# Optimization experiments

Hardware: AMD Instinct MI355X
Metric: run time of the kernel (lower is better)

## Reference

```python
import jax, jax.numpy as jnp
from jax import lax
import numpy as np

B, S, D, H = 64, 256, 1024, 1024
NEG = -1e9


def setup_inputs() -> dict:
    key = jax.random.key(0)
    ks = jax.random.split(key, 8)
    sd = 1.0 / np.sqrt(D)
    sh = 1.0 / np.sqrt(H + 1)
    return {
        "lstm_features": jax.random.normal(ks[0], (B, S, D), jnp.float32),
        "mask": jnp.ones((B, S), jnp.int32),
        "Wl": jax.random.normal(ks[1], (D, H), jnp.float32) * sd,
        "bl": jnp.zeros((H,), jnp.float32),
        "Wr": jax.random.normal(ks[2], (D, H), jnp.float32) * sd,
        "br": jnp.zeros((H,), jnp.float32),
        "Wbil": jax.random.normal(ks[3], (H + 1, H + 1), jnp.float32) * sh,
        "bbil": jnp.zeros((), jnp.float32),
    }


def _span_scores(lstm_features, Wl, bl, Wr, br, Wbil, bbil):
    # left/right MLPs: Linear + LeakyReLU(0.1) (dropout=0 at inference)
    lefts = jax.nn.leaky_relu(lstm_features @ Wl + bl, 0.1)   # [B,S,H]
    rights = jax.nn.leaky_relu(lstm_features @ Wr + br, 0.1)  # [B,S,H]
    ones = jnp.ones(lefts.shape[:-1] + (1,), lefts.dtype)
    l1 = jnp.concatenate([lefts, ones], axis=-1)   # [B,S,H+1] (use_input_biases=True)
    r1 = jnp.concatenate([rights, ones], axis=-1)
    # bilinear: l1 @ W @ r1^T + bias  -> [B,S,S]
    return jnp.einsum('bsh,hg,btg->bst', l1, Wbil, r1) + bbil


def _cky(scores):
    """CKY over one [S,S] score matrix. chart[i,j]=scores[i,j]+max_s chart[i,s]+chart[s+1,j];
    singleton spans score 0. Returns (chart, best-split table)."""
    n = scores.shape[0]
    idx = jnp.arange(n)
    m = jnp.arange(n - 1)  # split offsets
    chart0 = jnp.zeros((n, n), scores.dtype)
    split0 = jnp.zeros((n, n), jnp.int32)

    def step(carry, w):
        chart, split = carry
        j = idx + w
        jc = jnp.clip(j, 0, n - 1)
        li = jnp.clip(idx[:, None] + m[None, :], 0, n - 1)       # left end
        ri = jnp.clip(idx[:, None] + m[None, :] + 1, 0, n - 1)   # right start
        cand = chart[idx[:, None], li] + chart[ri, jc[:, None]]  # [n, n-1]
        valid = (m[None, :] < w) & (j[:, None] < n)
        cand = jnp.where(valid, cand, NEG)
        val = scores[idx, jc] + jnp.max(cand, axis=1)
        bsplit = (idx + jnp.argmax(cand, axis=1)).astype(jnp.int32)
        ok = j < n
        chart = chart.at[idx, jc].set(jnp.where(ok, val, chart[idx, jc]))
        split = split.at[idx, jc].set(jnp.where(ok, bsplit, split[idx, jc]))
        return (chart, split), None

    (chart, split), _ = lax.scan(step, (chart0, split0), jnp.arange(1, n))
    return chart, split


def _backtrack(split):
    """Extract the n-1 internal spans of the best tree (fixed-size stack, jit-safe)."""
    n = split.shape[0]
    stack = jnp.full((2 * n, 2), -1, jnp.int32).at[0].set(jnp.array([0, n - 1], jnp.int32))
    out = jnp.zeros((n, 2), jnp.int32)

    def body(t, state):
        def do_pop(st):
            stack, top, out, cnt = st
            ij = stack[top - 1]
            i, j = ij[0], ij[1]
            top = top - 1
            out = out.at[cnt].set(ij)
            cnt = cnt + 1
            s = split[i, j]
            stack = stack.at[top].set(jnp.stack([i, s]))          # left child
            top = top + (s > i).astype(jnp.int32)
            stack = stack.at[top].set(jnp.stack([s + 1, j]))      # right child
            top = top + (j > s + 1).astype(jnp.int32)
            return (stack, top, out, cnt)
        return lax.cond(state[1] > 0, do_pop, lambda s: s, state)

    state = (stack, jnp.int32(1), out, jnp.int32(0))
    _, _, out, _ = lax.fori_loop(0, n - 1, body, state)
    return out  # [n,2] (lefts, rights), zero-padded like torch.zeros in original


def reference(lstm_features, mask, Wl, bl, Wr, br, Wbil, bbil):
    scores = _span_scores(lstm_features, Wl, bl, Wr, br, Wbil, bbil)  # [B,S,S]
    _, split = jax.vmap(_cky)(scores)
    spans = jax.vmap(_backtrack)(split)  # [B,S,2]
    ret_lefts = spans[..., 0].astype(jnp.int64)
    ret_rights = spans[..., 1].astype(jnp.int64)
    return ret_lefts, ret_rights
```

## Files before the change

### kernel.cpp

```cpp
#include <hip/hip_runtime.h>
#include <cstdint>


#define Bb 64
#define Ss 256
#define Dd 1024
#define Hh 1024

typedef __attribute__((ext_vector_type(8))) _Float16 f16x8;
typedef __attribute__((ext_vector_type(4))) float f32x4;

__device__ __forceinline__ void split2(float x, unsigned short& h,
                                       unsigned short& l) {
  _Float16 hh = (_Float16)x;
  _Float16 ll = (_Float16)(x - (float)hh);
  h = __builtin_bit_cast(unsigned short, hh);
  l = __builtin_bit_cast(unsigned short, ll);
}

__global__ __launch_bounds__(256) void splitw_kernel(
    const float* __restrict__ W, int ldw, unsigned short* __restrict__ O,
    long long plane) {
  int idx = blockIdx.x * 256 + threadIdx.x;
  int n = idx >> 10, k = idx & 1023;
  float x = W[(long long)k * ldw + n];
  unsigned short h, l;
  split2(x, h, l);
  O[idx] = h;
  O[plane + idx] = l;
}

__global__ __launch_bounds__(256) void bilvec_kernel(
    const float* __restrict__ Wbil, float* __restrict__ brow,
    float* __restrict__ bcol, float* __restrict__ corner) {
  int i = blockIdx.x * 256 + threadIdx.x;
  brow[i] = Wbil[1024 * 1025 + i];
  bcol[i] = Wbil[i * 1025 + 1024];
  if (i == 0) corner[0] = Wbil[1024 * 1025 + 1024];
}

__device__ __forceinline__ void pack8(char* dst, const unsigned short* v) {
  uint4 u;
  u.x = (unsigned)v[0] | ((unsigned)v[1] << 16);
  u.y = (unsigned)v[2] | ((unsigned)v[3] << 16);
  u.z = (unsigned)v[4] | ((unsigned)v[5] << 16);
  u.w = (unsigned)v[6] | ((unsigned)v[7] << 16);
  *(uint4*)dst = u;
}

__device__ __forceinline__ void split_store16f(const float* xs, char* lds,
                                               int base, int wa0, int wa1) {
  unsigned short hs[16], ls[16];
#pragma unroll
  for (int i = 0; i < 16; ++i) split2(xs[i], hs[i], ls[i]);
  pack8(&lds[base + wa0], hs);
  pack8(&lds[base + wa1], hs + 8);
  pack8(&lds[base + 8192 + wa0], ls);
  pack8(&lds[base + 8192 + wa1], ls + 8);
}

#define MFMA4(afv, bh, blv, accs, nf)                                        \
  {                                                                          \
    _Pragma("unroll") for (int mf = 0; mf < 4; ++mf) accs[mf][nf] =          \
        __builtin_amdgcn_mfma_f32_16x16x32_f16(afv[0][mf], bh,               \
                                               accs[mf][nf], 0, 0, 0);       \
    _Pragma("unroll") for (int mf = 0; mf < 4; ++mf) accs[mf][nf] =          \
        __builtin_amdgcn_mfma_f32_16x16x32_f16(afv[0][mf], blv,              \
                                               accs[mf][nf], 0, 0, 0);       \
    _Pragma("unroll") for (int mf = 0; mf < 4; ++mf) accs[mf][nf] =          \
        __builtin_amdgcn_mfma_f32_16x16x32_f16(afv[1][mf], bh,               \
                                               accs[mf][nf], 0, 0, 0);       \
    _Pragma("unroll") for (int mf = 0; mf < 4; ++mf) accs[mf][nf] =          \
        __builtin_amdgcn_mfma_f32_16x16x32_f16(afv[1][mf], blv,              \
                                               accs[mf][nf], 0, 0, 0);       \
  }

template <bool LEAKY>
__global__ __launch_bounds__(256, 3) void gemm_mfma_kernel(
    const float* __restrict__ A, const unsigned short* __restrict__ Bsp,
    long long bplane, float* __restrict__ C0, float* __restrict__ C1,
    const float* __restrict__ bias0, const float* __restrict__ bias1) {
  const int m0 = blockIdx.y * 128;
  const int n0 = blockIdx.x * 128;
  __shared__ __align__(16) char lds[32768];
  const int t = threadIdx.x;
  const int L = t & 63, w = t >> 6, q = L >> 4, l15 = L & 15;

  const int ar = t >> 1, ah = t & 1;
  const float* aptr = A + (long long)(m0 + ar) * 1024 + ah * 16;
  const int phiA = ((ar >> 1) ^ (ar >> 3)) & 3;
  const int wa0 = ar * 64 + (((2 * ah + 0) ^ phiA) << 4);
  const int wa1 = ar * 64 + (((2 * ah + 1) ^ phiA) << 4);

  int offA0[4], offB0[4];
#pragma unroll
  for (int f = 0; f < 4; ++f) {
    int rowa = ((w & 1) << 6) + (f << 4) + l15;
    offA0[f] = rowa * 64 + ((q ^ (((rowa >> 1) ^ (rowa >> 3)) & 3)) << 4);
    int rowb = ((w >> 1) << 6) + (f << 4) + l15;
    offB0[f] =
        16384 + rowb * 64 + ((q ^ (((rowb >> 1) ^ (rowb >> 3)) & 3)) << 4);
  }

  f32x4 acc[4][4];
#pragma unroll
  for (int i = 0; i < 4; ++i)
#pragma unroll
    for (int j = 0; j < 4; ++j) acc[i][j] = (f32x4){0.f, 0.f, 0.f, 0.f};

  for (int k0 = 0; k0 < 1024; k0 += 32) {
#pragma unroll
    for (int j = 0; j < 4; ++j) {
      int fc = t + (j << 8);
      int s = fc >> 9, r = (fc >> 2) & 127, sc = fc & 3;
      const unsigned short* bs = Bsp + s * bplane;
      uint4 bv =
          *(const uint4*)(bs + (long long)(n0 + r) * 1024 + k0 + (sc << 3));
      int phi = ((r >> 1) ^ (r >> 3)) & 3;
      *(uint4*)&lds[16384 + s * 8192 + r * 64 + ((sc ^ phi) << 4)] = bv;
    }
    {
      float4 a0 = *(const float4*)(aptr + k0);
      float4 a1 = *(const float4*)(aptr + k0 + 4);
      float4 a2 = *(const float4*)(aptr + k0 + 8);
      float4 a3 = *(const float4*)(aptr + k0 + 12);
      float xs[16] = {a0.x, a0.y, a0.z, a0.w, a1.x, a1.y, a1.z, a1.w,
                      a2.x, a2.y, a2.z, a2.w, a3.x, a3.y, a3.z, a3.w};
      split_store16f(xs, lds, 0, wa0, wa1);
    }
    __syncthreads();
    f16x8 af[2][4];
#pragma unroll
    for (int s = 0; s < 2; ++s)
#pragma unroll
      for (int f = 0; f < 4; ++f)
        af[s][f] = *(const f16x8*)&lds[s * 8192 + offA0[f]];
#pragma unroll
    for (int nf = 0; nf < 4; ++nf) {
      f16x8 bh = *(const f16x8*)&lds[offB0[nf]];
      f16x8 bl = *(const f16x8*)&lds[8192 + offB0[nf]];
      MFMA4(af, bh, bl, acc, nf);
    }
    __syncthreads();
  }

  const bool isR = (n0 >= 1024);
  float* Co = isR ? C1 : C0;
  const float* bp = isR ? bias1 : bias0;
  const int nc0 = n0 & 1023;
#pragma unroll
  for (int nf = 0; nf < 4; ++nf) {
    int col = nc0 + ((w >> 1) << 6) + (nf << 4) + l15;
    float bz = bp[col];
#pragma unroll
    for (int mf = 0; mf < 4; ++mf) {
#pragma unroll
      for (int r = 0; r < 4; ++r) {
        int row = m0 + ((w & 1) << 6) + (mf << 4) + (q << 2) + r;
        float x = acc[mf][nf][r] + bz;
        if (LEAKY) x = (x > 0.f) ? x : 0.1f * x;
        Co[(long long)row * 1024 + col] = x;
      }
    }
  }
}

__global__ __launch_bounds__(256, 3) void gemmnt_mfma_kernel(
    const float* __restrict__ A, const float* __restrict__ B,
    float* __restrict__ C, const float* __restrict__ rowAdd,
    const float* __restrict__ scal) {
  const int bz = blockIdx.z;
  A += (long long)bz * 256 * 1024;
  B += (long long)bz * 256 * 1024;
  C += (long long)bz * 256 * 256;
  const int m0 = blockIdx.y * 128;
  const int n0 = blockIdx.x * 128;
  __shared__ __align__(16) char lds[32768];
  const int t = threadIdx.x;
  const int L = t & 63, w = t >> 6, q = L >> 4, l15 = L & 15;

  const int ar = t >> 1, ah = t & 1;
  const float* aptr = A + (long long)(m0 + ar) * 1024 + ah * 16;
  const float* bptr = B + (long long)(n0 + ar) * 1024 + ah * 16;
  const int phiA = ((ar >> 1) ^ (ar >> 3)) & 3;
  const int wa0 = ar * 64 + (((2 * ah + 0) ^ phiA) << 4);
  const int wa1 = ar * 64 + (((2 * ah + 1) ^ phiA) << 4);

  int offA0[4], offB0[4];
#pragma unroll
  for (int f = 0; f < 4; ++f) {
    int rowa = ((w & 1) << 6) + (f << 4) + l15;
    offA0[f] = rowa * 64 + ((q ^ (((rowa >> 1) ^ (rowa >> 3)) & 3)) << 4);
    int rowb = ((w >> 1) << 6) + (f << 4) + l15;
    offB0[f] =
        16384 + rowb * 64 + ((q ^ (((rowb >> 1) ^ (rowb >> 3)) & 3)) << 4);
  }

  f32x4 acc[4][4];
#pragma unroll
  for (int i = 0; i < 4; ++i)
#pragma unroll
    for (int j = 0; j < 4; ++j) acc[i][j] = (f32x4){0.f, 0.f, 0.f, 0.f};

  for (int k0 = 0; k0 < 1024; k0 += 32) {
    {
      float4 a0 = *(const float4*)(aptr + k0);
      float4 a1 = *(const float4*)(aptr + k0 + 4);
      float4 a2 = *(const float4*)(aptr + k0 + 8);
      float4 a3 = *(const float4*)(aptr + k0 + 12);
      float xs[16] = {a0.x, a0.y, a0.z, a0.w, a1.x, a1.y, a1.z, a1.w,
                      a2.x, a2.y, a2.z, a2.w, a3.x, a3.y, a3.z, a3.w};
      split_store16f(xs, lds, 0, wa0, wa1);
      float4 b0 = *(const float4*)(bptr + k0);
      float4 b1 = *(const float4*)(bptr + k0 + 4);
      float4 b2 = *(const float4*)(bptr + k0 + 8);
      float4 b3 = *(const float4*)(bptr + k0 + 12);
      float ys[16] = {b0.x, b0.y, b0.z, b0.w, b1.x, b1.y, b1.z, b1.w,
                      b2.x, b2.y, b2.z, b2.w, b3.x, b3.y, b3.z, b3.w};
      split_store16f(ys, lds, 16384, wa0, wa1);
    }
    __syncthreads();
    f16x8 af[2][4];
#pragma unroll
    for (int s = 0; s < 2; ++s)
#pragma unroll
      for (int f = 0; f < 4; ++f)
        af[s][f] = *(const f16x8*)&lds[s * 8192 + offA0[f]];
#pragma unroll
    for (int nf = 0; nf < 4; ++nf) {
      f16x8 bh = *(const f16x8*)&lds[offB0[nf]];
      f16x8 bl = *(const f16x8*)&lds[8192 + offB0[nf]];
      MFMA4(af, bh, bl, acc, nf);
    }
    __syncthreads();
  }

  const float sc_add = scal[0];
#pragma unroll
  for (int mf = 0; mf < 4; ++mf) {
#pragma unroll
    for (int r = 0; r < 4; ++r) {
      int row = m0 + ((w & 1) << 6) + (mf << 4) + (q << 2) + r;
      float radd = sc_add + rowAdd[(long long)bz * 256 + row];
#pragma unroll
      for (int nf = 0; nf < 4; ++nf) {
        int col = n0 + ((w >> 1) << 6) + (nf << 4) + l15;
        C[(long long)row * 256 + col] = acc[mf][nf][r] + radd;
      }
    }
  }
}

__global__ __launch_bounds__(64) void colvec_kernel(
    const float* __restrict__ lefts, const float* __restrict__ bcol,
    const float* __restrict__ corner, float* __restrict__ tmpb) {
  int row = blockIdx.x;
  int lane = threadIdx.x;
  const float* a = lefts + (long long)row * Hh;
  float s = 0.f;
#pragma unroll
  for (int h = lane; h < Hh; h += 64) s = fmaf(a[h], bcol[h], s);
#pragma unroll
  for (int off = 32; off > 0; off >>= 1) s += __shfl_down(s, off, 64);
  if (lane == 0) tmpb[row] = s + corner[0];
}

__global__ __launch_bounds__(1024) void cky_kernel(
    const float* __restrict__ scores,
    uint8_t* __restrict__ Sws,
    int* __restrict__ out)
{
  const int b = blockIdx.x;
  const int t = threadIdx.x;
  const int n = Ss;
  const float* sc = scores + (long long)b * n * n;
  uint8_t* SP = Sws + (long long)b * 32896;

  __shared__ float Dch[32896];
  __shared__ float pv[2][2048];
  __shared__ uint8_t pmv[2][2048];
  __shared__ int stk[256];

  const int offT[10] = {0,    256,  511,  765,  1018,
                        1270, 1521, 1771, 2020, 2268};

  if (t < n) {
    out[b * n + t] = 0;
    out[Bb * n + b * n + t] = 0;
    Dch[t] = 0.f;
  }

  float PS[10];
  PS[0] = 0.f;
#pragma unroll
  for (int w = 1; w <= 9; ++w) {
    int ic = t;
    if (ic > 255 - w) ic = 255 - w;
    PS[w] = sc[ic * 257 + w];
  }
  asm volatile("s_waitcnt lgkmcnt(0)\n\ts_barrier" ::: "memory");

#pragma unroll
  for (int w = 1; w <= 9; ++w) {
    const int nv = n - w;
    if (t < nv) {
      float bb = Dch[offT[w - 1] + t + 1];
      int bm = 0;
#pragma unroll
      for (int m = 1; m < 9; ++m) {
        if (m >= w) break;
        float c = Dch[offT[m] + t] + Dch[offT[w - 1 - m] + t + m + 1];
        if (c > bb) { bb = c; bm = m; }
      }
      const int off = w * 256 - ((w * (w - 1)) >> 1);
      Dch[off + t] = PS[w] + bb;
      SP[off + t] = (uint8_t)bm;
    }
    asm volatile("s_waitcnt lgkmcnt(0)\n\ts_barrier" ::: "memory");
  }

  auto run_b = [&](int W0b, int pbuf) {
    const int cnv = n - W0b - 4;
    int jb, gb, u, delta, lgGHL, SLOTG;
    if (cnv > 128) {
      const int p = t >> 7;
      jb = 3 - (p >> 1);
      gb = 1 - (p & 1);
      u = t & 127;
      delta = 128;
      lgGHL = 1;
      SLOTG = 256;
    } else {
      const int wid = t >> 6;
      jb = 3 - (wid >> 2);
      gb = 3 - (wid & 3);
      u = t & 63;
      delta = (cnv > 64) ? 64 : 0;
      lgGHL = 2;
      SLOTG = 128;
    }
    const int Wb = W0b + 4 + jb;
    const int nvb = n - Wb;
    int cnt = W0b - jb - 4;
    if (cnt < 0) cnt = 0;
    const int per = (cnt + (1 << lgGHL) - 1) >> lgGHL;
    const int mlo = jb + 4;
    int ml = mlo + gb * per;
    int mh = mlo + cnt;
    {
      int e = ml + per;
      if (e < mh) mh = e;
    }
    float b0 = -3.0e38f, b1 = -3.0e38f;
    int m0i = ml, m1i = ml;
    if (u < nvb && ml < mh) {
      int al = ml * n - ((ml * (ml - 1)) >> 1) + u;
      const int kr = Wb - 1 - ml;
      int ar = kr * n - ((kr * (kr - 1)) >> 1) + u + ml + 1;
      int dl = n - ml;
      int dr = n - Wb + ml + 1;
      if (delta) {
#pragma unroll 2
        for (int m = ml; m < mh; ++m) {
          float l0 = Dch[al], l1 = Dch[al + delta];
          float r0 = Dch[ar], r1 = Dch[ar + delta];
          float c0 = l0 + r0, c1 = l1 + r1;
          if (c0 > b0) { b0 = c0; m0i = m; }
          if (c1 > b1) { b1 = c1; m1i = m; }
          al += dl;
          ar -= dr;
          --dl;
          ++dr;
        }
      } else {
#pragma unroll 4
        for (int m = ml; m < mh; ++m) {
          float c = Dch[al] + Dch[ar];
          if (c > b0) { b0 = c; m0i = m; }
          al += dl;
          ar -= dr;
          --dl;
          ++dr;
        }
      }
    }
    const int slot = jb * 512 + gb * SLOTG + u;
    pv[pbuf][slot] = b0;
    pmv[pbuf][slot] = (uint8_t)m0i;
    if (delta) {
      pv[pbuf][slot + delta] = b1;
      pmv[pbuf][slot + delta] = (uint8_t)m1i;
    }
  };

  run_b(6, 0);
  asm volatile("s_waitcnt lgkmcnt(0)\n\ts_barrier" ::: "memory");

  const int wv = t >> 6, lane = t & 63;
  const int tcell = 61 * wv + lane;

  float scA[4];
#pragma unroll
  for (int j = 0; j < 4; ++j) {
    const int Wn = 10 + j;
    int ic = tcell;
    if (ic > 255 - Wn) ic = 255 - Wn;
    if (ic < 0) ic = 0;
    scA[j] = sc[ic * 257 + Wn];
  }

  for (int s = 3; s <= 64; ++s) {
    const int W0 = 4 * s - 2;
    const int nv1 = n - W0;
    const int pb = s & 1, po = pb ^ 1;
    const int nb = (nv1 + 60) / 61;

    float P4[4] = {0.f, 0.f, 0.f, 0.f};
    if (s < 64 && wv < nb) {
#pragma unroll
      for (int j = 0; j < 4; ++j) {
        const int Wn = W0 + 4 + j;
        int ic = tcell;
        if (ic > 255 - Wn) ic = 255 - Wn;
        if (ic < 0) ic = 0;
        P4[j] = sc[ic * 257 + Wn];
      }
    }

    if (wv < nb) {
      const int tc = (tcell < nv1) ? tcell : (nv1 - 1);
      const float* pvo = pv[po];
      const uint8_t* pmo = pmv[po];
      int GHa, SGa;
      if (nv1 > 128) { GHa = 2; SGa = 256; } else { GHa = 4; SGa = 128; }
      int offPB[4], offCB[4];
#pragma unroll
      for (int d = 0; d < 4; ++d) {
        const int dg = W0 - 4 + d;
        offPB[d] = dg * 256 - ((dg * (dg - 1)) >> 1);
        const int cg = W0 + d;
        offCB[d] = cg * 256 - ((cg * (cg - 1)) >> 1);
      }
      float VAL0, VAL1, VAL2, VAL3;
      float SH01, SH02, SH03, SH11, SH12, SH21;
      {
        const int W = W0;
        float bb = Dch[offPB[3] + tc + 1];
        int bm = 0;
#pragma unroll
        for (int dm = 1; dm < 4; ++dm) {
          const int m = dm;
          float c = Dch[offT[m] + tc] + Dch[offPB[3 - dm] + tc + m + 1];
          if (c > bb) { bb = c; bm = m; }
        }
#pragma unroll
        for (int g = 0; g < 4; ++g) {
          if (g >= GHa) break;
          const int sl = g * SGa + tc;
          float x = pvo[sl];
          if (x > bb) { bb = x; bm = pmo[sl]; }
        }
#pragma unroll
        for (int dr = 3; dr >= 0; --dr) {
          const int r = dr;
          const int m = W - 1 - r;
          float right = (r == 0) ? 0.f : Dch[offT[r] + tc + W - r];
          float c = Dch[offPB[3 - dr] + tc] + right;
          if (c > bb) { bb = c; bm = m; }
        }
        VAL0 = scA[0] + bb;
        if (tcell < nv1) {
          Dch[offCB[0] + tcell] = VAL0;
          SP[offCB[0] + tcell] = (uint8_t)bm;
        }
        SH01 = __shfl_down(VAL0, 1, 64);
        SH02 = __shfl_down(VAL0, 2, 64);
        SH03 = __shfl_down(VAL0, 3, 64);
      }
      {
        const int W = W0 + 1;
        float bb = SH01;
        int bm = 0;
#pragma unroll
        for (int dm = 0; dm < 4; ++dm) {
          const int m = 1 + dm;
          float c = Dch[offT[m] + tc] + Dch[offPB[3 - dm] + tc + m + 1];
          if (c > bb) { bb = c; bm = m; }
        }
#pragma unroll
        for (int g = 0; g < 4; ++g) {
          if (g >= GHa) break;
          const int sl = 512 + g * SGa + tc;
          float x = pvo[sl];
          if (x > bb) { bb = x; bm = pmo[sl]; }
        }
#pragma unroll
        for (int dr = 3; dr >= 0; --dr) {
          const int r = 1 + dr;
          const int m = W - 1 - r;
          float c = Dch[offPB[3 - dr] + tc] + Dch[offT[r] + tc + W - r];
          if (c > bb) { bb = c; bm = m; }
        }
        if (VAL0 > bb) { bb = VAL0; bm = W - 1; }
        VAL1 = scA[1] + bb;
        if (lane <= 62 && tcell < nv1 - 1) {
          Dch[offCB[1] + tcell] = VAL1;
          SP[offCB[1] + tcell] = (uint8_t)bm;
        }
        SH11 = __shfl_down(VAL1, 1, 64);
        SH12 = __shfl_down(VAL1, 2, 64);
      }
      {
        const int W = W0 + 2;
        float bb = SH11;
        int bm = 0;
        {
          float c = Dch[offT[1] + tc] + SH02;
          if (c > bb) { bb = c; bm = 1; }
        }
#pragma unroll
        for (int dm = 0; dm < 4; ++dm) {
          const int m = 2 + dm;
          float c = Dch[offT[m] + tc] + Dch[offPB[3 - dm] + tc + m + 1];
          if (c > bb) { bb = c; bm = m; }
        }
#pragma unroll
        for (int g = 0; g < 4; ++g) {
          if (g >= GHa) break;
          const int sl = 1024 + g * SGa + tc;
          float x = pvo[sl];
          if (x > bb) { bb = x; bm = pmo[sl]; }
        }
#pragma unroll
        for (int dr = 3; dr >= 0; --dr) {
          const int r = 2 + dr;
          const int m = W - 1 - r;
          float c = Dch[offPB[3 - dr] + tc] + Dch[offT[r] + tc + W - r];
          if (c > bb) { bb = c; bm = m; }
        }
        {
          float c = VAL0 + Dch[offT[1] + tc + W - 1];
          if (c > bb) { bb = c; bm = W - 2; }
        }
        if (VAL1 > bb) { bb = VAL1; bm = W - 1; }
        VAL2 = scA[2] + bb;
        if (lane <= 61 && tcell < nv1 - 2) {
          Dch[offCB[2] + tcell] = VAL2;
          SP[offCB[2] + tcell] = (uint8_t)bm;
        }
        SH21 = __shfl_down(VAL2, 1, 64);
      }
      {
        const int W = W0 + 3;
        float bb = SH21;
        int bm = 0;
        {
          float c = Dch[offT[1] + tc] + SH12;
          if (c > bb) { bb = c; bm = 1; }
        }
        {
          float c = Dch[offT[2] + tc] + SH03;
          if (c > bb) { bb = c; bm = 2; }
        }
#pragma unroll
        for (int dm = 0; dm < 4; ++dm) {
          const int m = 3 + dm;
          float c = Dch[offT[m] + tc] + Dch[offPB[3 - dm] + tc + m + 1];
          if (c > bb) { bb = c; bm = m; }
        }
#pragma unroll
        for (int g = 0; g < 4; ++g) {
          if (g >= GHa) break;
          const int sl = 1536 + g * SGa + tc;
          float x = pvo[sl];
          if (x > bb) { bb = x; bm = pmo[sl]; }
        }
#pragma unroll
        for (int dr = 3; dr >= 0; --dr) {
          const int r = 3 + dr;
          const int m = W - 1 - r;
          float c = Dch[offPB[3 - dr] + tc] + Dch[offT[r] + tc + W - r];
          if (c > bb) { bb = c; bm = m; }
        }
        {
          float c = VAL0 + Dch[offT[2] + tc + W - 2];
          if (c > bb) { bb = c; bm = W - 3; }
        }
        {
          float c = VAL1 + Dch[offT[1] + tc + W - 1];
          if (c > bb) { bb = c; bm = W - 2; }
        }
        if (VAL2 > bb) { bb = VAL2; bm = W - 1; }
        VAL3 = scA[3] + bb;
        if (lane <= 60 && tcell < nv1 - 3) {
          Dch[offCB[3] + tcell] = VAL3;
          SP[offCB[3] + tcell] = (uint8_t)bm;
        }
      }
    }

    if (s < 64) run_b(W0, pb);

    asm volatile("s_waitcnt lgkmcnt(0)\n\ts_barrier" ::: "memory");
#pragma unroll
    for (int j = 0; j < 4; ++j) scA[j] = P4[j];
  }

  asm volatile("s_waitcnt vmcnt(0) lgkmcnt(0)\n\ts_barrier" ::: "memory");
  uint8_t* spl = (uint8_t*)Dch;
  for (int idx = t; idx < 32896; idx += 1024) spl[idx] = SP[idx];
  asm volatile("s_waitcnt vmcnt(0) lgkmcnt(0)\n\ts_barrier" ::: "memory");
  if (t == 0) {
    int top = 0;
    stk[top++] = (0 << 16) | (n - 1);
    int cnt = 0;
    for (int step = 0; step < n - 1; ++step) {
      if (top > 0) {
        int ij = stk[--top];
        int ii = ij >> 16, jj = ij & 0xffff;
        out[b * n + cnt] = ii;
        out[Bb * n + b * n + cnt] = jj;
        ++cnt;
        int k = jj - ii;
        int s2 = ii + (int)spl[k * n - ((k * (k - 1)) >> 1) + ii];
        stk[top] = (ii << 16) | s2;
        if (s2 > ii) ++top;
        stk[top] = ((s2 + 1) << 16) | jj;
        if (jj > s2 + 1) ++top;
      }
    }
  }
}

extern "C" void kernel_launch(void* const* d_in, const int* in_sizes, int n_in,
                              void* d_out, int out_size, void* d_ws,
                              size_t ws_size, hipStream_t stream) {
  const float* X = (const float*)d_in[0];
  const float* Wl = (const float*)d_in[2];
  const float* bl = (const float*)d_in[3];
  const float* Wr = (const float*)d_in[4];
  const float* br = (const float*)d_in[5];
  const float* Wbil = (const float*)d_in[6];
  const float* bbil = (const float*)d_in[7];
  int* out = (int*)d_out;

  float* ws = (float*)d_ws;
  float* lefts = ws;
  float* rights = lefts + 16777216;
  float* tmpA = rights + 16777216;
  float* scoresP = tmpA + 16777216;
  float* tmpb = scoresP + 4194304;
  float* browp = tmpb + 16384;
  float* bcolp = browp + 1024;
  float* cornerp = bcolp + 1024;
  unsigned short* Wlrt = (unsigned short*)(cornerp + 4);
  unsigned short* Wct = Wlrt + 2LL * 2097152;
  uint8_t* SPp = (uint8_t*)(Wct + 2LL * 1048576);

  splitw_kernel<<<dim3(4096), 256, 0, stream>>>(Wl, 1024, Wlrt, 2097152);
  splitw_kernel<<<dim3(4096), 256, 0, stream>>>(Wr, 1024, Wlrt + 1048576,
                                                2097152);
  splitw_kernel<<<dim3(4096), 256, 0, stream>>>(Wbil, 1025, Wct, 1048576);
  bilvec_kernel<<<dim3(4), 256, 0, stream>>>(Wbil, browp, bcolp, cornerp);

  dim3 gLR(16, 128);
  gemm_mfma_kernel<true><<<gLR, 256, 0, stream>>>(X, Wlrt, 2097152LL, lefts,
                                                  rights, bl, br);

  colvec_kernel<<<dim3(16384), 64, 0, stream>>>(lefts, bcolp, cornerp, tmpb);

  dim3 gA(8, 128);
  gemm_mfma_kernel<false><<<gA, 256, 0, stream>>>(lefts, Wct, 1048576LL, tmpA,
                                                  tmpA, browp, browp);

  dim3 g3(2, 2, 64);
  gemmnt_mfma_kernel<<<g3, 256, 0, stream>>>(tmpA, rights, scoresP, tmpb,
                                             bbil);

  cky_kernel<<<dim3(Bb), dim3(1024), 0, stream>>>(scoresP, SPp, out);
}
```

Baseline: 943.7 us.

## Prefetch next K-tile in GEMMs via direct global-to-LDS loads and double buffering

In the projection GEMM, the pre-split fp16 B tiles now go straight from global memory to LDS through global_load_lds into a double-buffered region. The fp32 A tile for the next k-step is prefetched into registers while MFMAs run on the current one. The bilinear GEMM gets the same register prefetch for both operands. Plain __syncthreads is replaced with explicit waitcnt plus s_barrier so load latency overlaps compute. LDS use grows from 32KB to 48KB, which may lower occupancy relative to the launch-bounds target of 3 blocks per CU.

```diff
diff --git a/kernel.cpp b/kernel.cpp
--- a/kernel.cpp
+++ b/kernel.cpp
@@ -16,6 +16,12 @@
   _Float16 ll = (_Float16)(x - (float)hh);
   h = __builtin_bit_cast(unsigned short, hh);
   l = __builtin_bit_cast(unsigned short, ll);
+}
+
+__device__ __forceinline__ void gl_lds16(const void* g, void* l) {
+  __builtin_amdgcn_global_load_lds(
+      (const __attribute__((address_space(1))) void*)g,
+      (__attribute__((address_space(3))) void*)l, 16, 0, 0);
 }
 
 __global__ __launch_bounds__(256) void splitw_kernel(
@@ -82,7 +88,7 @@
     const float* __restrict__ bias0, const float* __restrict__ bias1) {
   const int m0 = blockIdx.y * 128;
   const int n0 = blockIdx.x * 128;
-  __shared__ __align__(16) char lds[32768];
+  __shared__ __align__(16) char lds[49152];
   const int t = threadIdx.x;
   const int L = t & 63, w = t >> 6, q = L >> 4, l15 = L & 15;
 
@@ -98,8 +104,21 @@
     int rowa = ((w & 1) << 6) + (f << 4) + l15;
     offA0[f] = rowa * 64 + ((q ^ (((rowa >> 1) ^ (rowa >> 3)) & 3)) << 4);
     int rowb = ((w >> 1) << 6) + (f << 4) + l15;
-    offB0[f] =
-        16384 + rowb * 64 + ((q ^ (((rowb >> 1) ^ (rowb >> 3)) & 3)) << 4);
+    offB0[f] = rowb * 64 + ((q ^ (((rowb >> 1) ^ (rowb >> 3)) & 3)) << 4);
+  }
+
+  const int lrow = L >> 2, lchk = L & 3;
+  const unsigned short* bsrc[4];
+  int bldso[4];
+#pragma unroll
+  for (int i = 0; i < 4; ++i) {
+    int O = ((w << 2) + i) << 10;
+    int s2 = O >> 13;
+    int r = ((O & 8191) >> 6) + lrow;
+    int phi = ((r >> 1) ^ (r >> 3)) & 3;
+    bsrc[i] = Bsp + (long long)s2 * bplane + (long long)(n0 + r) * 1024 +
+              ((lchk ^ phi) << 3);
+    bldso[i] = O;
   }
 
   f32x4 acc[4][4];
@@ -108,27 +127,32 @@
 #pragma unroll
     for (int j = 0; j < 4; ++j) acc[i][j] = (f32x4){0.f, 0.f, 0.f, 0.f};
 
+#pragma unroll
+  for (int i = 0; i < 4; ++i) gl_lds16(bsrc[i], &lds[16384 + bldso[i]]);
+  float4 a0 = *(const float4*)(aptr + 0);
+  float4 a1 = *(const float4*)(aptr + 4);
+  float4 a2 = *(const float4*)(aptr + 8);
+  float4 a3 = *(const float4*)(aptr + 12);
+
+  int cur = 0;
   for (int k0 = 0; k0 < 1024; k0 += 32) {
-#pragma unroll
-    for (int j = 0; j < 4; ++j) {
-      int fc = t + (j << 8);
-      int s = fc >> 9, r = (fc >> 2) & 127, sc = fc & 3;
-      const unsigned short* bs = Bsp + s * bplane;
-      uint4 bv =
-          *(const uint4*)(bs + (long long)(n0 + r) * 1024 + k0 + (sc << 3));
-      int phi = ((r >> 1) ^ (r >> 3)) & 3;
-      *(uint4*)&lds[16384 + s * 8192 + r * 64 + ((sc ^ phi) << 4)] = bv;
-    }
     {
-      float4 a0 = *(const float4*)(aptr + k0);
-      float4 a1 = *(const float4*)(aptr + k0 + 4);
-      float4 a2 = *(const float4*)(aptr + k0 + 8);
-      float4 a3 = *(const float4*)(aptr + k0 + 12);
       float xs[16] = {a0.x, a0.y, a0.z, a0.w, a1.x, a1.y, a1.z, a1.w,
                       a2.x, a2.y, a2.z, a2.w, a3.x, a3.y, a3.z, a3.w};
       split_store16f(xs, lds, 0, wa0, wa1);
     }
-    __syncthreads();
+    asm volatile("s_waitcnt vmcnt(0) lgkmcnt(0)\n\ts_barrier" ::: "memory");
+    if (k0 < 992) {
+      a0 = *(const float4*)(aptr + k0 + 32);
+      a1 = *(const float4*)(aptr + k0 + 36);
+      a2 = *(const float4*)(aptr + k0 + 40);
+      a3 = *(const float4*)(aptr + k0 + 44);
+      const int bn = 16384 + ((cur ^ 1) << 14);
+#pragma unroll
+      for (int i = 0; i < 4; ++i)
+        gl_lds16(bsrc[i] + k0 + 32, &lds[bn + bldso[i]]);
+    }
+    const int bb = 16384 + (cur << 14);
     f16x8 af[2][4];
 #pragma unroll
     for (int s = 0; s < 2; ++s)
@@ -137,11 +161,12 @@
         af[s][f] = *(const f16x8*)&lds[s * 8192 + offA0[f]];
 #pragma unroll
     for (int nf = 0; nf < 4; ++nf) {
-      f16x8 bh = *(const f16x8*)&lds[offB0[nf]];
-      f16x8 bl = *(const f16x8*)&lds[8192 + offB0[nf]];
+      f16x8 bh = *(const f16x8*)&lds[bb + offB0[nf]];
+      f16x8 bl = *(const f16x8*)&lds[bb + 8192 + offB0[nf]];
       MFMA4(af, bh, bl, acc, nf);
     }
-    __syncthreads();
+    asm volatile("s_waitcnt lgkmcnt(0)\n\ts_barrier" ::: "memory");
+    cur ^= 1;
   }
 
   const bool isR = (n0 >= 1024);
@@ -202,24 +227,35 @@
 #pragma unroll
     for (int j = 0; j < 4; ++j) acc[i][j] = (f32x4){0.f, 0.f, 0.f, 0.f};
 
+  float4 a0 = *(const float4*)(aptr + 0);
+  float4 a1 = *(const float4*)(aptr + 4);
+  float4 a2 = *(const float4*)(aptr + 8);
+  float4 a3 = *(const float4*)(aptr + 12);
+  float4 b0 = *(const float4*)(bptr + 0);
+  float4 b1 = *(const float4*)(bptr + 4);
+  float4 b2 = *(const float4*)(bptr + 8);
+  float4 b3 = *(const float4*)(bptr + 12);
+
   for (int k0 = 0; k0 < 1024; k0 += 32) {
     {
-      float4 a0 = *(const float4*)(aptr + k0);
-      float4 a1 = *(const float4*)(aptr + k0 + 4);
-      float4 a2 = *(const float4*)(aptr + k0 + 8);
-      float4 a3 = *(const float4*)(aptr + k0 + 12);
       float xs[16] = {a0.x, a0.y, a0.z, a0.w, a1.x, a1.y, a1.z, a1.w,
                       a2.x, a2.y, a2.z, a2.w, a3.x, a3.y, a3.z, a3.w};
       split_store16f(xs, lds, 0, wa0, wa1);
-      float4 b0 = *(const float4*)(bptr + k0);
-      float4 b1 = *(const float4*)(bptr + k0 + 4);
-      float4 b2 = *(const float4*)(bptr + k0 + 8);
-      float4 b3 = *(const float4*)(bptr + k0 + 12);
       float ys[16] = {b0.x, b0.y, b0.z, b0.w, b1.x, b1.y, b1.z, b1.w,
                       b2.x, b2.y, b2.z, b2.w, b3.x, b3.y, b3.z, b3.w};
       split_store16f(ys, lds, 16384, wa0, wa1);
     }
-    __syncthreads();
+    asm volatile("s_waitcnt lgkmcnt(0)\n\ts_barrier" ::: "memory");
+    if (k0 < 992) {
+      a0 = *(const float4*)(aptr + k0 + 32);
+      a1 = *(const float4*)(aptr + k0 + 36);
+      a2 = *(const float4*)(aptr + k0 + 40);
+      a3 = *(const float4*)(aptr + k0 + 44);
+      b0 = *(const float4*)(bptr + k0 + 32);
+      b1 = *(const float4*)(bptr + k0 + 36);
+      b2 = *(const float4*)(bptr + k0 + 40);
+      b3 = *(const float4*)(bptr + k0 + 44);
+    }
     f16x8 af[2][4];
 #pragma unroll
     for (int s = 0; s < 2; ++s)
@@ -232,7 +268,7 @@
       f16x8 bl = *(const f16x8*)&lds[8192 + offB0[nf]];
       MFMA4(af, bh, bl, acc, nf);
     }
-    __syncthreads();
+    asm volatile("s_waitcnt lgkmcnt(0)\n\ts_barrier" ::: "memory");
   }
 
   const float sc_add = scal[0];
```

After: 865.2 us. -8.3%, faster.
